# Kernel tuning notes

Measured on AMD Instinct MI355X. Metric: run time of the kernel, lower is better.

## Reference

```python
import jax, jax.numpy as jnp
import numpy as np

NEG_SLOPE = 0.2  # PyG GATConv leaky_relu slope
EPS = 1e-16


def gat_layer(x, W, att_src, att_dst, bias, src, dst, num_nodes, heads, out_c, concat):
    # x: [N, F_in], W: [F_in, heads*out_c], att_*: [heads, out_c], bias: [heads*out_c] or [out_c]
    xp = (x @ W).reshape(num_nodes, heads, out_c)              # [N, H, C]
    a_src = (xp * att_src).sum(-1)                             # [N, H]
    a_dst = (xp * att_dst).sum(-1)                             # [N, H]
    alpha = jax.nn.leaky_relu(a_src[src] + a_dst[dst], NEG_SLOPE)  # [E, H]
    # segment softmax over destination-node neighborhoods
    m = jax.ops.segment_max(alpha, dst, num_segments=num_nodes)   # [N, H]
    e = jnp.exp(alpha - m[dst])
    s = jax.ops.segment_sum(e, dst, num_segments=num_nodes)
    alpha = e / (s[dst] + EPS)                                 # [E, H]
    out = jax.ops.segment_sum(xp[src] * alpha[:, :, None], dst, num_segments=num_nodes)  # [N, H, C]
    out = out.reshape(num_nodes, heads * out_c) if concat else out.mean(axis=1)
    return out + bias


def setup_inputs() -> dict:
    key = jax.random.key(0)
    N, E, F = 100000, 3200000, 128
    ks = jax.random.split(key, 10)
    x = jax.random.normal(ks[0], (N, F), dtype=jnp.float32)
    edge_index = jax.random.randint(ks[1], (2, E), 0, N, dtype=jnp.int64)
    s1 = 1.0 / np.sqrt(F)
    W1 = jax.random.normal(ks[2], (F, 2 * 16), dtype=jnp.float32) * s1
    att_src1 = jax.random.normal(ks[3], (2, 16), dtype=jnp.float32) * 0.25
    att_dst1 = jax.random.normal(ks[4], (2, 16), dtype=jnp.float32) * 0.25
    b1 = jnp.zeros((32,), dtype=jnp.float32)
    W2 = jax.random.normal(ks[5], (32, 1), dtype=jnp.float32) * (1.0 / np.sqrt(32))
    att_src2 = jax.random.normal(ks[6], (1, 1), dtype=jnp.float32)
    att_dst2 = jax.random.normal(ks[7], (1, 1), dtype=jnp.float32)
    b2 = jnp.zeros((1,), dtype=jnp.float32)
    return {"x": x, "edge_index": edge_index, "W1": W1, "att_src1": att_src1,
            "att_dst1": att_dst1, "b1": b1, "W2": W2, "att_src2": att_src2,
            "att_dst2": att_dst2, "b2": b2}


def reference(x, edge_index, W1, att_src1, att_dst1, b1, W2, att_src2, att_dst2, b2):
    N = x.shape[0]
    # PyG GATConv adds self-loops by default
    loops = jnp.arange(N, dtype=edge_index.dtype)
    src = jnp.concatenate([edge_index[0], loops])
    dst = jnp.concatenate([edge_index[1], loops])
    h = gat_layer(x, W1, att_src1, att_dst1, b1, src, dst, N, 2, 16, True)   # [N, 32]
    h = jax.nn.relu(h)
    out = gat_layer(h, W2, att_src2, att_dst2, b2, src, dst, N, 1, 1, False)  # [N, 1]
    return out.sum(axis=0, keepdims=True)  # [1, 1]
```

## Files before the change

kernel.cpp:

```cpp
#include <hip/hip_runtime.h>
#include <hip/hip_bf16.h>
#include <hip/hip_fp16.h>
#include <hip/hip_fp8.h>
#include <math.h>

#define NEG_SLOPE 0.2f
#define EPS 1e-16f
#define CHUNK 4096
#define BSH 8
#define BNODES 256

__device__ __forceinline__ float leaky(float x) {
    return x > 0.f ? x : NEG_SLOPE * x;
}

__device__ __forceinline__ int block_scan_excl_1024(int v, int t, int* waveS) {
    int lane = t & 63, w = t >> 6;
    int inc = v;
#pragma unroll
    for (int off = 1; off < 64; off <<= 1) {
        int u = __shfl_up(inc, off);
        if (lane >= off) inc += u;
    }
    if (lane == 63) waveS[w] = inc;
    __syncthreads();
    if (w == 0) {
        int s = (lane < 16) ? waveS[lane] : 0;
#pragma unroll
        for (int off = 1; off < 16; off <<= 1) {
            int u = __shfl_up(s, off);
            if (lane >= off) s += u;
        }
        if (lane < 16) waveS[lane] = s;
    }
    __syncthreads();
    int base = (w > 0) ? waveS[w - 1] : 0;
    return base + inc - v;
}

__global__ __launch_bounds__(1024) void chunkhist_kernel(
    const int* __restrict__ ei, int E, int ET, int NB, int NC,
    int* __restrict__ cnt) {
    __shared__ int histL[1024];
    int t = threadIdx.x;
    int c = blockIdx.x;
    if (t < NB) histL[t] = 0;
    __syncthreads();
    int e0 = c * CHUNK;
#pragma unroll 4
    for (int i = t; i < CHUNK; i += 1024) {
        int e = e0 + i;
        if (e < ET) {
            int d = (e < E) ? ei[E + e] : (e - E);
            atomicAdd(&histL[d >> BSH], 1);
        }
    }
    __syncthreads();
    if (t < NB) cnt[(size_t)t * NC + c] = histL[t];
}

__global__ void scan_block(const int* __restrict__ in, int* __restrict__ out,
                           int* __restrict__ partials, int n) {
    __shared__ int waveS[16];
    int t = threadIdx.x;
    int g = blockIdx.x * 1024 + t;
    int v = (g < n) ? in[g] : 0;
    int ex = block_scan_excl_1024(v, t, waveS);
    if (g < n) out[g] = ex;
    if (t == 0) partials[blockIdx.x] = waveS[15];
}

__global__ void scan_partials(int* __restrict__ partials, int P) {
    __shared__ int waveS[16];
    int t = threadIdx.x;
    int v = (t < P) ? partials[t] : 0;
    int ex = block_scan_excl_1024(v, t, waveS);
    if (t < P) partials[t] = ex;
}

__device__ __forceinline__ int gscan(const int* scanned, const int* partials,
                                     size_t g) {
    return scanned[g] + partials[g >> 10];
}

__global__ __launch_bounds__(1024) void packsort_kernel(
    const int* __restrict__ ei, int E, int ET, int NB, int NC,
    const int* __restrict__ scanned, const int* __restrict__ partials,
    unsigned int* __restrict__ packed) {
    __shared__ unsigned int sortedL[CHUNK];
    __shared__ int gposL[CHUNK];
    __shared__ int histL[1024];
    __shared__ int cursorL[1024];
    __shared__ int diffL[1024];
    __shared__ int waveS[16];
    int t = threadIdx.x;
    int c = blockIdx.x;
    int e0 = c * CHUNK;
    int cw = ET - e0; if (cw > CHUNK) cw = CHUNK;

    if (t < NB) histL[t] = 0;
    __syncthreads();

    unsigned int pk[4]; int bb[4];
#pragma unroll
    for (int k = 0; k < 4; k++) {
        int i = t + k * 1024;
        bb[k] = -1;
        if (i < cw) {
            int e = e0 + i;
            int s, d;
            if (e < E) { s = ei[e]; d = ei[E + e]; } else { s = d = e - E; }
            bb[k] = d >> BSH;
            pk[k] = ((unsigned int)s << BSH) | (unsigned int)(d & (BNODES - 1));
            atomicAdd(&histL[bb[k]], 1);
        }
    }
    __syncthreads();
    int hv = (t < NB) ? histL[t] : 0;
    int ex = block_scan_excl_1024(hv, t, waveS);
    if (t < NB) {
        cursorL[t] = ex;
        size_t g = (size_t)t * NC + c;
        diffL[t] = gscan(scanned, partials, g) - ex;
    }
    __syncthreads();
#pragma unroll
    for (int k = 0; k < 4; k++) {
        if (bb[k] >= 0) {
            int lpos = atomicAdd(&cursorL[bb[k]], 1);
            sortedL[lpos] = pk[k];
            gposL[lpos] = diffL[bb[k]] + lpos;
        }
    }
    __syncthreads();
    for (int i = t; i < cw; i += 1024)
        packed[gposL[i]] = sortedL[i];
}

__global__ __launch_bounds__(1024) void localsort_kernel(
    const unsigned int* __restrict__ packed, const int* __restrict__ scanned,
    const int* __restrict__ partials, int NB, int NC, int ET,
    int* __restrict__ srt, int* __restrict__ binptr, int N) {
    __shared__ int histL[BNODES];
    __shared__ int curL[BNODES];
    __shared__ int waveS[16];
    int t = threadIdx.x;
    int bkt = blockIdx.x;
    int base = bkt * BNODES;
    int ebeg = gscan(scanned, partials, (size_t)bkt * NC);
    int eend = (bkt + 1 < NB) ? gscan(scanned, partials, (size_t)(bkt + 1) * NC) : ET;
    if (t < BNODES) histL[t] = 0;
    __syncthreads();
    for (int i = ebeg + t; i < eend; i += 1024)
        atomicAdd(&histL[packed[i] & (BNODES - 1)], 1);
    __syncthreads();
    int hv = (t < BNODES) ? histL[t] : 0;
    int ex = block_scan_excl_1024(hv, t, waveS);
    if (t < BNODES) {
        curL[t] = ex;
        int gn = base + t;
        if (gn < N) binptr[gn] = ebeg + ex;
    }
    if (bkt == 0 && t == 0) binptr[N] = ET;
    __syncthreads();
    for (int i = ebeg + t; i < eend; i += 1024) {
        unsigned int p = packed[i];
        int dl = p & (BNODES - 1);
        int pos = ebeg + atomicAdd(&curL[dl], 1);
        srt[pos] = (int)(p >> BSH);
    }
}

__device__ __forceinline__ void fma4(float4& acc, float sc, const float4& wv) {
    acc.x = fmaf(sc, wv.x, acc.x);
    acc.y = fmaf(sc, wv.y, acc.y);
    acc.z = fmaf(sc, wv.z, acc.z);
    acc.w = fmaf(sc, wv.w, acc.w);
}

__global__ __launch_bounds__(256) void gemm1_kernel(
    const float* __restrict__ x, const float* __restrict__ W1,
    const float4* __restrict__ att_src4, const float4* __restrict__ att_dst4,
    unsigned int* __restrict__ xp1u, float* __restrict__ a_src,
    float* __restrict__ a_dst, int N) {
    __shared__ float4 wS4[128 * 8];
    __shared__ float4 xS4[64 * 32];
    int t = threadIdx.x;
    int base = blockIdx.x * 64;
#pragma unroll
    for (int i = 0; i < 4; i++)
        wS4[t + i * 256] = ((const float4*)W1)[t + i * 256];
#pragma unroll
    for (int i = 0; i < 8; i++) {
        int idx = t + i * 256;
        int row = idx >> 5, kb = idx & 31;
        xS4[idx] = (base + row < N) ? ((const float4*)x)[(size_t)(base + row) * 32 + kb]
                                    : make_float4(0.f, 0.f, 0.f, 0.f);
    }
    __syncthreads();

    int cq = t & 7;
    int rg = t >> 3;
    const float4* xr0 = xS4 + (rg * 2) * 32;
    const float4* xr1 = xr0 + 32;
    float4 a0 = make_float4(0.f, 0.f, 0.f, 0.f);
    float4 a1 = make_float4(0.f, 0.f, 0.f, 0.f);
#pragma unroll 4
    for (int kb = 0; kb < 32; kb++) {
        float4 x0 = xr0[kb];
        float4 x1 = xr1[kb];
        float4 w0 = wS4[(kb * 4 + 0) * 8 + cq];
        float4 w1 = wS4[(kb * 4 + 1) * 8 + cq];
        float4 w2 = wS4[(kb * 4 + 2) * 8 + cq];
        float4 w3 = wS4[(kb * 4 + 3) * 8 + cq];
        fma4(a0, x0.x, w0); fma4(a0, x0.y, w1); fma4(a0, x0.z, w2); fma4(a0, x0.w, w3);
        fma4(a1, x1.x, w0); fma4(a1, x1.y, w1); fma4(a1, x1.z, w2); fma4(a1, x1.w, w3);
    }

    float4 asv = att_src4[cq];
    float4 adv = att_dst4[cq];
    int r0 = base + rg * 2, r1 = r0 + 1;
    float va0 = a0.x * asv.x + a0.y * asv.y + a0.z * asv.z + a0.w * asv.w;
    float vd0 = a0.x * adv.x + a0.y * adv.y + a0.z * adv.z + a0.w * adv.w;
    float va1 = a1.x * asv.x + a1.y * asv.y + a1.z * asv.z + a1.w * asv.w;
    float vd1 = a1.x * adv.x + a1.y * adv.y + a1.z * adv.z + a1.w * adv.w;
#pragma unroll
    for (int off = 1; off <= 2; off <<= 1) {
        va0 += __shfl_xor(va0, off);
        vd0 += __shfl_xor(vd0, off);
        va1 += __shfl_xor(va1, off);
        vd1 += __shfl_xor(vd1, off);
    }
    if (r0 < N) {
        __hip_fp8x4_e4m3 q0(a0);
        xp1u[(size_t)r0 * 8 + cq] = *(unsigned int*)&q0;
        if ((cq & 3) == 0) {
            int h = cq >> 2;
            a_src[r0 * 2 + h] = va0;
            a_dst[r0 * 2 + h] = vd0;
        }
    }
    if (r1 < N) {
        __hip_fp8x4_e4m3 q1(a1);
        xp1u[(size_t)r1 * 8 + cq] = *(unsigned int*)&q1;
        if ((cq & 3) == 0) {
            int h = cq >> 2;
            a_src[r1 * 2 + h] = va1;
            a_dst[r1 * 2 + h] = vd1;
        }
    }
}

#define AGG1_CONSUME(KN)                                                        \
    _Pragma("unroll")                                                           \
    for (int k = 0; k < KN; k++) {                                              \
        float4 st = stage[wib][k * 8 + eg];                                     \
        int sk = __float_as_int(st.x);                                          \
        float ek = hsel ? st.z : st.y;                                          \
        unsigned int u = *(const unsigned int*)(xpb + (size_t)sk * 32);         \
        float4 xv = (float4)(*reinterpret_cast<const __hip_fp8x4_e4m3*>(&u));   \
        acc0 = fmaf(ek, xv.x, acc0);                                            \
        acc1 = fmaf(ek, xv.y, acc1);                                            \
        acc2 = fmaf(ek, xv.z, acc2);                                            \
        acc3 = fmaf(ek, xv.w, acc3);                                            \
        ssum += ek;                                                             \
    }

__global__ __launch_bounds__(256) void agg1_kernel(
    const int* __restrict__ binptr, const int* __restrict__ srt,
    const float2* __restrict__ a_src2, const float2* __restrict__ a_dst2,
    const unsigned char* __restrict__ xp1f8, const float* __restrict__ b1,
    const float* __restrict__ W2, float* __restrict__ xp2, int N) {
    __shared__ float4 stage[4][64];
    int tg = blockIdx.x * blockDim.x + threadIdx.x;
    int n = tg >> 6;
    int lane = threadIdx.x & 63;
    int wib = threadIdx.x >> 6;
    if (n >= N) return;
    int eg = lane >> 3;
    int cq = lane & 7;
    int hsel = cq >> 2;
    int beg = binptr[n], end = binptr[n + 1];
    float2 ad = a_dst2[n];
    const unsigned char* xpb = xp1f8 + cq * 4;

    float acc0 = 0.f, acc1 = 0.f, acc2 = 0.f, acc3 = 0.f, ssum = 0.f;
    for (int i0 = beg; i0 < end; i0 += 64) {
        int cw = end - i0;
        if (cw > 64) cw = 64;
        if (lane < cw) {
            int s_l = srt[i0 + lane];
            float2 as = a_src2[s_l];
            stage[wib][lane] = make_float4(__int_as_float(s_l),
                                           __expf(leaky(as.x + ad.x)),
                                           __expf(leaky(as.y + ad.y)), 0.f);
        } else {
            stage[wib][lane] = make_float4(0.f, 0.f, 0.f, 0.f);
        }
        if (cw > 48)      { AGG1_CONSUME(8) }
        else if (cw > 32) { AGG1_CONSUME(6) }
        else if (cw > 16) { AGG1_CONSUME(4) }
        else              { AGG1_CONSUME(2) }
    }
#pragma unroll
    for (int off = 8; off <= 32; off <<= 1) {
        acc0 += __shfl_xor(acc0, off);
        acc1 += __shfl_xor(acc1, off);
        acc2 += __shfl_xor(acc2, off);
        acc3 += __shfl_xor(acc3, off);
        ssum += __shfl_xor(ssum, off);
    }
    float inv = 1.f / (ssum + EPS);
    int j0 = cq * 4;
    float p;
    {
        float hv0 = fmaxf(acc0 * inv + b1[j0 + 0], 0.f);
        float hv1 = fmaxf(acc1 * inv + b1[j0 + 1], 0.f);
        float hv2 = fmaxf(acc2 * inv + b1[j0 + 2], 0.f);
        float hv3 = fmaxf(acc3 * inv + b1[j0 + 3], 0.f);
        p = hv0 * W2[j0 + 0];
        p = fmaf(hv1, W2[j0 + 1], p);
        p = fmaf(hv2, W2[j0 + 2], p);
        p = fmaf(hv3, W2[j0 + 3], p);
    }
    p += __shfl_xor(p, 1);
    p += __shfl_xor(p, 2);
    p += __shfl_xor(p, 4);
    if (lane == 0) xp2[n] = p;
}

__global__ __launch_bounds__(256) void agg2_kernel(
    const int* __restrict__ binptr, const int* __restrict__ srt,
    const float* __restrict__ xp2, const float* __restrict__ as2p,
    const float* __restrict__ ad2p, const float* __restrict__ b2,
    float* __restrict__ partial, int N) {
    int slot = (blockIdx.x * blockDim.x + threadIdx.x) >> 5;
    int j = threadIdx.x & 31;
    int nslots = (gridDim.x * blockDim.x) >> 5;
    float as2 = as2p[0], ad2 = ad2p[0], bb = b2[0];
    float val = 0.f;
    for (int n = slot; n < N; n += nslots) {
        int beg = binptr[n], end = binptr[n + 1];
        float xd = xp2[n] * ad2;
        float se = 0.f, sa = 0.f;
        for (int i = beg + j; i < end; i += 32) {
            float xs = xp2[srt[i]];
            float ex = __expf(leaky(fmaf(xs, as2, xd)));
            se += ex;
            sa = fmaf(ex, xs, sa);
        }
#pragma unroll
        for (int off = 16; off >= 1; off >>= 1) {
            se += __shfl_xor(se, off);
            sa += __shfl_xor(sa, off);
        }
        if (j == 0) val += sa / (se + EPS) + bb;
    }
#pragma unroll
    for (int off = 32; off >= 1; off >>= 1) val += __shfl_xor(val, off);
    __shared__ float ls[4];
    int lane = threadIdx.x & 63, w = threadIdx.x >> 6;
    if (lane == 0) ls[w] = val;
    __syncthreads();
    if (threadIdx.x == 0) partial[blockIdx.x] = ls[0] + ls[1] + ls[2] + ls[3];
}

__global__ void final_reduce(const float* __restrict__ partial, float* __restrict__ out,
                             int P) {
    int t = threadIdx.x;
    float v = 0.f;
    for (int i = t; i < P; i += 1024) v += partial[i];
#pragma unroll
    for (int off = 32; off >= 1; off >>= 1) v += __shfl_xor(v, off);
    __shared__ float ls[16];
    int w = t >> 6, lane = t & 63;
    if (lane == 0) ls[w] = v;
    __syncthreads();
    if (t == 0) {
        float s = 0.f;
        for (int i = 0; i < 16; i++) s += ls[i];
        out[0] = s;
    }
}

extern "C" void kernel_launch(void* const* d_in, const int* in_sizes, int n_in,
                              void* d_out, int out_size, void* d_ws, size_t ws_size,
                              hipStream_t stream) {
    const float* x        = (const float*)d_in[0];
    const int*   ei       = (const int*)d_in[1];
    const float* W1       = (const float*)d_in[2];
    const float* att_src1 = (const float*)d_in[3];
    const float* att_dst1 = (const float*)d_in[4];
    const float* b1       = (const float*)d_in[5];
    const float* W2       = (const float*)d_in[6];
    const float* att_src2 = (const float*)d_in[7];
    const float* att_dst2 = (const float*)d_in[8];
    const float* b2       = (const float*)d_in[9];
    float* out = (float*)d_out;

    int N = in_sizes[0] / 128;
    int E = in_sizes[1] / 2;
    int ET = E + N;
    int NB = (N + BNODES - 1) / BNODES;
    int NC = (ET + CHUNK - 1) / CHUNK;
    int n_scan = NB * NC;
    int nb2 = (n_scan + 1023) / 1024;
    const int AGG2_BLOCKS = 2048;

    char* w = (char*)d_ws;
    unsigned char* xp1f8 = (unsigned char*)w; w += (size_t)N * 32;
    float* a_src   = (float*)w;  w += sizeof(float) * (size_t)N * 2;
    float* a_dst   = (float*)w;  w += sizeof(float) * (size_t)N * 2;
    float* xp2     = (float*)w;  w += sizeof(float) * (size_t)N;
    int* cnt       = (int*)w;    w += sizeof(int) * (size_t)n_scan;
    int* scanned   = (int*)w;    w += sizeof(int) * (size_t)(n_scan + 4);
    int* partials  = (int*)w;    w += sizeof(int) * 1024;
    float* part2   = (float*)w;  w += sizeof(float) * (size_t)AGG2_BLOCKS;
    unsigned int* packed = (unsigned int*)w; w += sizeof(unsigned int) * (size_t)ET;
    int* srt       = (int*)w;    w += sizeof(int) * (size_t)ET;
    int* binptr    = (int*)w;    w += sizeof(int) * (size_t)(N + 1);

    gemm1_kernel<<<(N + 63) / 64, 256, 0, stream>>>(x, W1,
                                                    (const float4*)att_src1,
                                                    (const float4*)att_dst1,
                                                    (unsigned int*)xp1f8, a_src,
                                                    a_dst, N);
    chunkhist_kernel<<<NC, 1024, 0, stream>>>(ei, E, ET, NB, NC, cnt);
    scan_block<<<nb2, 1024, 0, stream>>>(cnt, scanned, partials, n_scan);
    scan_partials<<<1, 1024, 0, stream>>>(partials, nb2);
    packsort_kernel<<<NC, 1024, 0, stream>>>(ei, E, ET, NB, NC, scanned, partials,
                                             packed);
    localsort_kernel<<<NB, 1024, 0, stream>>>(packed, scanned, partials, NB, NC, ET,
                                              srt, binptr, N);
    agg1_kernel<<<(N * 64 + 255) / 256, 256, 0, stream>>>(binptr, srt,
                                                          (const float2*)a_src,
                                                          (const float2*)a_dst,
                                                          xp1f8, b1, W2, xp2, N);
    agg2_kernel<<<AGG2_BLOCKS, 256, 0, stream>>>(binptr, srt, xp2,
                                                 att_src2, att_dst2, b2, part2, N);
    final_reduce<<<1, 1024, 0, stream>>>(part2, out, AGG2_BLOCKS);
}
```

Baseline: 154.5 us.

## Replace LDS staging with shuffles, pack weights as bf16, interleave two nodes in agg2

In the first aggregation kernel, the per-wave shared-memory stage of (src, exp weights) is replaced by register broadcasts via __shfl, and the two head weights are packed as rounded bf16 halves in one 32-bit word. The fp8x4 decode now uses the cvt_pk_f32_fp8 builtin when it is available. The second aggregation kernel processes two destination nodes per 32-lane group at once, which raises the number of independent gathers in flight. The changes trade LDS traffic and barrier-free staging for shuffle instructions, and they cut the precision of the softmax weights to bf16. That precision loss could shift accuracy slightly.

```diff
diff --git a/kernel.cpp b/kernel.cpp
--- a/kernel.cpp
+++ b/kernel.cpp
@@ -9,6 +9,26 @@
 #define CHUNK 4096
 #define BSH 8
 #define BNODES 256
+
+typedef float floatx2 __attribute__((ext_vector_type(2)));
+
+#if defined(__has_builtin)
+# if __has_builtin(__builtin_amdgcn_cvt_pk_f32_fp8)
+#  define USE_CVT_BUILTIN 1
+# endif
+#endif
+
+__device__ __forceinline__ void fp8x4_to_f32(unsigned int u, float& f0, float& f1,
+                                             float& f2, float& f3) {
+#ifdef USE_CVT_BUILTIN
+    floatx2 lo = __builtin_amdgcn_cvt_pk_f32_fp8(u, false);
+    floatx2 hi = __builtin_amdgcn_cvt_pk_f32_fp8(u, true);
+    f0 = lo.x; f1 = lo.y; f2 = hi.x; f3 = hi.y;
+#else
+    float4 xv = (float4)(*reinterpret_cast<const __hip_fp8x4_e4m3*>(&u));
+    f0 = xv.x; f1 = xv.y; f2 = xv.z; f3 = xv.w;
+#endif
+}
 
 __device__ __forceinline__ float leaky(float x) {
     return x > 0.f ? x : NEG_SLOPE * x;
@@ -254,15 +274,17 @@
 #define AGG1_CONSUME(KN)                                                        \
     _Pragma("unroll")                                                           \
     for (int k = 0; k < KN; k++) {                                              \
-        float4 st = stage[wib][k * 8 + eg];                                     \
-        int sk = __float_as_int(st.x);                                          \
-        float ek = hsel ? st.z : st.y;                                          \
+        int es = k * 8 + eg;                                                    \
+        int sk = __shfl(s_l, es);                                               \
+        unsigned int pw = (unsigned int)__shfl((int)pk_l, es);                  \
+        float ek = __uint_as_float(hsel ? (pw & 0xFFFF0000u) : (pw << 16));     \
         unsigned int u = *(const unsigned int*)(xpb + (size_t)sk * 32);         \
-        float4 xv = (float4)(*reinterpret_cast<const __hip_fp8x4_e4m3*>(&u));   \
-        acc0 = fmaf(ek, xv.x, acc0);                                            \
-        acc1 = fmaf(ek, xv.y, acc1);                                            \
-        acc2 = fmaf(ek, xv.z, acc2);                                            \
-        acc3 = fmaf(ek, xv.w, acc3);                                            \
+        float f0, f1, f2, f3;                                                   \
+        fp8x4_to_f32(u, f0, f1, f2, f3);                                        \
+        acc0 = fmaf(ek, f0, acc0);                                              \
+        acc1 = fmaf(ek, f1, acc1);                                              \
+        acc2 = fmaf(ek, f2, acc2);                                              \
+        acc3 = fmaf(ek, f3, acc3);                                              \
         ssum += ek;                                                             \
     }
 
@@ -271,11 +293,9 @@
     const float2* __restrict__ a_src2, const float2* __restrict__ a_dst2,
     const unsigned char* __restrict__ xp1f8, const float* __restrict__ b1,
     const float* __restrict__ W2, float* __restrict__ xp2, int N) {
-    __shared__ float4 stage[4][64];
     int tg = blockIdx.x * blockDim.x + threadIdx.x;
     int n = tg >> 6;
     int lane = threadIdx.x & 63;
-    int wib = threadIdx.x >> 6;
     if (n >= N) return;
     int eg = lane >> 3;
     int cq = lane & 7;
@@ -288,14 +308,15 @@
     for (int i0 = beg; i0 < end; i0 += 64) {
         int cw = end - i0;
         if (cw > 64) cw = 64;
+        int s_l = 0;
+        unsigned int pk_l = 0u;
         if (lane < cw) {
-            int s_l = srt[i0 + lane];
+            s_l = srt[i0 + lane];
             float2 as = a_src2[s_l];
-            stage[wib][lane] = make_float4(__int_as_float(s_l),
-                                           __expf(leaky(as.x + ad.x)),
-                                           __expf(leaky(as.y + ad.y)), 0.f);
-        } else {
-            stage[wib][lane] = make_float4(0.f, 0.f, 0.f, 0.f);
+            float e0 = __expf(leaky(as.x + ad.x));
+            float e1 = __expf(leaky(as.y + ad.y));
+            pk_l = ((__float_as_uint(e1) + 0x8000u) & 0xFFFF0000u) |
+                   ((__float_as_uint(e0) + 0x8000u) >> 16);
         }
         if (cw > 48)      { AGG1_CONSUME(8) }
         else if (cw > 32) { AGG1_CONSUME(6) }
@@ -339,22 +360,43 @@
     int nslots = (gridDim.x * blockDim.x) >> 5;
     float as2 = as2p[0], ad2 = ad2p[0], bb = b2[0];
     float val = 0.f;
-    for (int n = slot; n < N; n += nslots) {
-        int beg = binptr[n], end = binptr[n + 1];
-        float xd = xp2[n] * ad2;
-        float se = 0.f, sa = 0.f;
-        for (int i = beg + j; i < end; i += 32) {
-            float xs = xp2[srt[i]];
-            float ex = __expf(leaky(fmaf(xs, as2, xd)));
-            se += ex;
-            sa = fmaf(ex, xs, sa);
+    for (int n0 = slot; n0 < N; n0 += 2 * nslots) {
+        int n1 = n0 + nslots;
+        bool has1 = n1 < N;
+        int beg0 = binptr[n0], end0 = binptr[n0 + 1];
+        int beg1 = has1 ? binptr[n1] : 0;
+        int end1 = has1 ? binptr[n1 + 1] : 0;
+        float xd0 = xp2[n0] * ad2;
+        float xd1 = has1 ? xp2[n1] * ad2 : 0.f;
+        float se0 = 0.f, sa0 = 0.f, se1 = 0.f, sa1 = 0.f;
+        int it0 = (end0 - beg0 - j + 31) >> 5;
+        int it1 = (end1 - beg1 - j + 31) >> 5;
+        int itm = it0 > it1 ? it0 : it1;
+        for (int k = 0; k < itm; k++) {
+            int i0 = beg0 + j + k * 32;
+            int i1 = beg1 + j + k * 32;
+            if (i0 < end0) {
+                float xs = xp2[srt[i0]];
+                float ex = __expf(leaky(fmaf(xs, as2, xd0)));
+                se0 += ex; sa0 = fmaf(ex, xs, sa0);
+            }
+            if (has1 && i1 < end1) {
+                float xs = xp2[srt[i1]];
+                float ex = __expf(leaky(fmaf(xs, as2, xd1)));
+                se1 += ex; sa1 = fmaf(ex, xs, sa1);
+            }
         }
 #pragma unroll
         for (int off = 16; off >= 1; off >>= 1) {
-            se += __shfl_xor(se, off);
-            sa += __shfl_xor(sa, off);
-        }
-        if (j == 0) val += sa / (se + EPS) + bb;
+            se0 += __shfl_xor(se0, off);
+            sa0 += __shfl_xor(sa0, off);
+            se1 += __shfl_xor(se1, off);
+            sa1 += __shfl_xor(sa1, off);
+        }
+        if (j == 0) {
+            val += sa0 / (se0 + EPS) + bb;
+            if (has1) val += sa1 / (se1 + EPS) + bb;
+        }
     }
 #pragma unroll
     for (int off = 32; off >= 1; off >>= 1) val += __shfl_xor(val, off);
```

Result: faster. 150.8 us (-2.4%).
